# Performance work log

Hardware: AMD Instinct MI355X
Metric: run time of the kernel (lower is better)

Reference implementation:

```python
import jax, jax.numpy as jnp
import numpy as np

NEG_CAUSAL = -1e10  # matches torch buffer triu(ones*-1e10, diag=1)
NEG_PAD = -10000.0
NUM_HEADS = 16


def setup_inputs() -> dict:
    key = jax.random.key(0)
    ks = jax.random.split(key, 6)
    B, S, D = 2, 2048, 1024
    scale = 0.02
    return {
        "hidden_states": jax.random.normal(ks[0], (B, S, D), jnp.float32),
        "attention_mask": jnp.ones((B, S), jnp.float32),
        "Wq": jax.random.normal(ks[1], (D, D), jnp.float32) * scale,
        "bq": jnp.zeros((D,), jnp.float32),
        "Wk": jax.random.normal(ks[2], (D, D), jnp.float32) * scale,
        "bk": jnp.zeros((D,), jnp.float32),
        "Wv": jax.random.normal(ks[3], (D, D), jnp.float32) * scale,
        "bv": jnp.zeros((D,), jnp.float32),
        "Wo": jax.random.normal(ks[4], (D, D), jnp.float32) * scale,
        "bo": jnp.zeros((D,), jnp.float32),
    }


def reference(hidden_states, attention_mask, Wq, bq, Wk, bk, Wv, bv, Wo, bo):
    B, S, D = hidden_states.shape
    H = NUM_HEADS
    hd = D // H

    def heads(x):  # [B,S,D] -> [B,H,S,hd]
        return x.reshape(B, S, H, hd).transpose(0, 2, 1, 3)

    q = heads(hidden_states @ Wq + bq)
    k = heads(hidden_states @ Wk + bk)
    v = heads(hidden_states @ Wv + bv)

    scores = jnp.einsum("bhqd,bhkd->bhqk", q, k) / jnp.sqrt(jnp.float32(hd))
    causal = jnp.triu(jnp.full((S, S), NEG_CAUSAL, jnp.float32), k=1)
    scores = scores + causal
    # additive padding mask: (1 - m) * -10000, broadcast over heads and query pos
    scores = scores + (1.0 - attention_mask)[:, None, None, :] * NEG_PAD

    probs = jax.nn.softmax(scores, axis=-1)
    # dropout p=0.1 is inactive in eval mode (training=False)
    ctx = jnp.einsum("bhqk,bhkd->bhqd", probs, v)
    ctx = ctx.transpose(0, 2, 1, 3).reshape(B, S, D)
    return ctx @ Wo + bo
```

## Files before the change

kernel.cpp:

```cpp
#include <hip/hip_runtime.h>

typedef __attribute__((ext_vector_type(8))) short short8_t;
typedef __attribute__((ext_vector_type(4))) float float4_t;
typedef unsigned short u16;
typedef unsigned int u32;
typedef unsigned long long u64;

__device__ inline u16 f2bf(float x) {
  union { float f; u32 u; } v; v.f = x;
  u32 r = v.u + 0x7FFFu + ((v.u >> 16) & 1u);
  return (u16)(r >> 16);
}
#if __has_builtin(__builtin_amdgcn_cvt_pk_bf16_f32)
typedef __attribute__((ext_vector_type(2))) __bf16 bf162_t;
__device__ inline u32 pk2(float a, float b) {
  union { bf162_t v; u32 u; } cv;
  cv.v = __builtin_amdgcn_cvt_pk_bf16_f32(a, b);
  return cv.u;
}
#else
__device__ inline u32 pk2(float a, float b) {
  return (u32)f2bf(a) | ((u32)f2bf(b) << 16);
}
#endif

__global__ __launch_bounds__(256) void prologue(const float* __restrict__ X,
                                                const float* __restrict__ Wq, const float* __restrict__ Wk,
                                                const float* __restrict__ Wv, const float* __restrict__ Wo,
                                                u16* __restrict__ Xb, u16* __restrict__ WqkvT,
                                                u16* __restrict__ WoT) {
  __shared__ float tls[32][33];
  int bid = blockIdx.x;
  if (bid < 4096) {
    int i = bid * 256 + threadIdx.x;
    float4_t x = ((const float4_t*)X)[i];
    union { u32 u[2]; u64 ll; } o;
    o.u[0] = pk2(x[0], x[1]);
    o.u[1] = pk2(x[2], x[3]);
    ((u64*)Xb)[i] = o.ll;
  } else {
    int t = bid - 4096;
    int mat = t >> 10, tile = t & 1023;
    const float* W = (mat == 0) ? Wq : (mat == 1) ? Wk : (mat == 2) ? Wv : Wo;
    u16* WT = (mat < 3) ? WqkvT + ((size_t)mat << 20) : WoT;
    int tx = threadIdx.x & 31, ty = threadIdx.x >> 5;
    int c0 = (tile & 31) * 32, r0 = (tile >> 5) * 32;
    #pragma unroll
    for (int i = 0; i < 4; ++i)
      tls[ty + i * 8][tx] = W[(r0 + ty + i * 8) * 1024 + c0 + tx];
    __syncthreads();
    #pragma unroll
    for (int i = 0; i < 4; ++i)
      WT[(size_t)(c0 + ty + i * 8) * 1024 + r0 + tx] = f2bf(tls[tx][ty + i * 8]);
  }
}

__global__ __launch_bounds__(256) void gemm128(const u16* __restrict__ A, const u16* __restrict__ BT,
                                               const float* __restrict__ bias0, const float* __restrict__ bias1,
                                               const float* __restrict__ bias2,
                                               void* __restrict__ o0, void* __restrict__ o1, void* __restrict__ o2,
                                               int mode) {
  __shared__ __align__(16) u16 Als[128 * 64];
  __shared__ __align__(16) u16 Bls[128 * 64];
  int g = blockIdx.x, m0t, n0t;
  if (mode == 4) {
    int mh = g / 384, r = g - mh * 384;
    n0t = r >> 4;
    m0t = mh * 16 + (r & 15);
  } else {
    m0t = g & 31;
    n0t = g >> 5;
  }
  const int m0 = m0t * 128, n0 = n0t * 128;
  const int lane = threadIdx.x & 63, wave = threadIdx.x >> 6;
  const int quad = lane >> 4, c = lane & 15;
  const int wm = wave >> 1, wn = wave & 1;

  const int srow = lane >> 3, schunk = lane & 7;
  int soff[4], dst[4];
  #pragma unroll
  for (int q = 0; q < 4; ++q) {
    int r = wave * 32 + q * 8 + srow;
    soff[q] = r * 1024 + (schunk << 3);
    dst[q]  = r * 64 + ((schunk ^ (r & 7)) << 3);
  }
  const u16* gA = A + (size_t)m0 * 1024;
  const u16* gB = BT + (size_t)n0 * 1024;

  int ar[2][4], br[2][4];
  #pragma unroll
  for (int ko = 0; ko < 2; ++ko) {
    #pragma unroll
    for (int i = 0; i < 4; ++i) {
      int rowa = wm * 64 + i * 16 + c;
      ar[ko][i] = rowa * 64 + (((ko * 4 + quad) ^ (rowa & 7)) << 3);
      int rowb = wn * 64 + i * 16 + c;
      br[ko][i] = rowb * 64 + (((ko * 4 + quad) ^ (rowb & 7)) << 3);
    }
  }

  short8_t ra[4], rb[4];
  #pragma unroll
  for (int q = 0; q < 4; ++q) ra[q] = *(const short8_t*)(gA + soff[q]);
  #pragma unroll
  for (int q = 0; q < 4; ++q) rb[q] = *(const short8_t*)(gB + soff[q]);

  float4_t acc[4][4] = {};
  for (int k0 = 0; k0 < 1024; k0 += 64) {
    #pragma unroll
    for (int q = 0; q < 4; ++q) *(short8_t*)&Als[dst[q]] = ra[q];
    #pragma unroll
    for (int q = 0; q < 4; ++q) *(short8_t*)&Bls[dst[q]] = rb[q];
    __syncthreads();
    if (k0 < 960) {
      #pragma unroll
      for (int q = 0; q < 4; ++q) ra[q] = *(const short8_t*)(gA + soff[q] + k0 + 64);
      #pragma unroll
      for (int q = 0; q < 4; ++q) rb[q] = *(const short8_t*)(gB + soff[q] + k0 + 64);
    }
    #pragma unroll
    for (int ko = 0; ko < 2; ++ko) {
      short8_t af[4], bfr[4];
      #pragma unroll
      for (int i = 0; i < 4; ++i) af[i] = *(const short8_t*)&Als[ar[ko][i]];
      #pragma unroll
      for (int j = 0; j < 4; ++j) bfr[j] = *(const short8_t*)&Bls[br[ko][j]];
      #pragma unroll
      for (int i = 0; i < 4; ++i)
        #pragma unroll
        for (int j = 0; j < 4; ++j)
          acc[i][j] = __builtin_amdgcn_mfma_f32_16x16x32_bf16(af[i], bfr[j], acc[i][j], 0, 0, 0);
    }
    __syncthreads();
  }

  const int mrow = m0 + wm * 64, ncol = n0 + wn * 64;
  if (mode == 3) {
    float* o = (float*)o0;
    #pragma unroll
    for (int i = 0; i < 4; ++i) {
      #pragma unroll
      for (int j = 0; j < 4; ++j) {
        int colb = ncol + j * 16 + c;
        float bv = bias0[colb];
        int rowb = mrow + i * 16 + quad * 4;
        #pragma unroll
        for (int r = 0; r < 4; ++r)
          o[(size_t)(rowb + r) * 1024 + colb] = acc[i][j][r] + bv;
      }
    }
  } else {
    #pragma unroll
    for (int j = 0; j < 4; ++j) {
      int colb = ncol + j * 16 + c;
      int which = colb >> 10;
      int n1 = colb & 1023, h = n1 >> 6, d = n1 & 63;
      const float* bp = (which == 0) ? bias0 : (which == 1 ? bias1 : bias2);
      float bv = bp[n1];
      #pragma unroll
      for (int i = 0; i < 4; ++i) {
        int rowb = mrow + i * 16 + quad * 4;
        int b = rowb >> 11, s = rowb & 2047;
        if (which == 2) {
          u16* o = (u16*)o2 + (((size_t)(b * 16 + h) * 64 + d) * 2048 + s);
          union { u32 u[2]; u64 ll; } ov;
          ov.u[0] = pk2(acc[i][j][0] + bv, acc[i][j][1] + bv);
          ov.u[1] = pk2(acc[i][j][2] + bv, acc[i][j][3] + bv);
          *(u64*)o = ov.ll;
        } else {
          float sc = (which == 0) ? 0.125f : 1.0f;
          u16* o = (u16*)((which == 0) ? o0 : o1);
          #pragma unroll
          for (int r = 0; r < 4; ++r)
            o[(((size_t)(b * 16 + h) * 2048 + (s + r)) << 6) + d] = f2bf((acc[i][j][r] + bv) * sc);
        }
      }
    }
  }
}

__device__ inline short8_t p_to_b32(const float* p, int quad, int c) {
  u32 pk0[2] = {pk2(p[0], p[1]), pk2(p[2], p[3])};
  u32 pk1[2] = {pk2(p[4], p[5]), pk2(p[6], p[7])};
  int base = ((quad & 1) * 2) * 16 + c;
  union { u32 u[4]; short8_t v; } pf;
  #pragma unroll
  for (int x = 0; x < 4; ++x) {
    int src = base + ((x >> 1) << 4);
    int v0 = __shfl((int)pk0[x & 1], src);
    int v1 = __shfl((int)pk1[x & 1], src);
    pf.u[x] = (quad < 2) ? (u32)v0 : (u32)v1;
  }
  return pf.v;
}

__global__ __launch_bounds__(256, 4) void attn_kernel(const u16* __restrict__ Q, const u16* __restrict__ K,
                                                      const u16* __restrict__ VT, const float* __restrict__ mask,
                                                      u16* __restrict__ ctx) {
  __shared__ __align__(16) u16 Kls[2 * 64 * 64];
  __shared__ __align__(16) u16 Vls[2 * 64 * 64];
  const float C1 = 10000.0f * 1.4426950408889634f;
  const float LOG2E = 1.4426950408889634f;
  int w = threadIdx.x >> 6, lane = threadIdx.x & 63;
  int quad = lane >> 4, c = lane & 15;
  int g = blockIdx.x;
  int bh = (g & 7) * 4 + ((g >> 3) & 3);
  int u = g >> 5;
  int qt = (u < 16) ? (31 - u) : (u - 16);
  int b = bh >> 4, h = bh & 15;
  const u16* Kp = K + ((size_t)bh << 17);
  const u16* Vp = VT + ((size_t)bh << 17);
  const float* mp = mask + (b << 11);
  int q0 = qt * 64 + w * 16;

  const u16* Qp = Q + (((size_t)bh * 2048 + q0 + c) << 6) + quad * 8;
  short8_t qf0 = *(const short8_t*)(Qp);
  short8_t qf1 = *(const short8_t*)(Qp + 32);

  const int srow = lane >> 3, schunk = lane & 7;
  const u16* gK[2]; const u16* gV[2]; int dK[2], dV[2];
  #pragma unroll
  for (int i = 0; i < 2; ++i) {
    int R = w * 16 + i * 8 + srow;
    gK[i] = Kp + R * 64 + (schunk << 3);
    dK[i] = R * 64 + ((schunk ^ (R & 7)) << 3);
    gV[i] = Vp + (size_t)R * 2048 + (schunk << 3);
    dV[i] = R * 64 + ((schunk ^ (R & 7)) << 3);
  }

  int koff[4][2];
  #pragma unroll
  for (int kg = 0; kg < 4; ++kg) {
    int r = kg * 16 + c;
    #pragma unroll
    for (int ko = 0; ko < 2; ++ko)
      koff[kg][ko] = r * 64 + (((ko * 4 + quad) ^ (r & 7)) << 3);
  }
  int voff[4][2];
  #pragma unroll
  for (int dblk = 0; dblk < 4; ++dblk) {
    int d = dblk * 16 + c;
    #pragma unroll
    for (int kc = 0; kc < 2; ++kc)
      voff[dblk][kc] = d * 64 + (((kc * 4 + quad) ^ (d & 7)) << 3);
  }

  int ke[8];
  #pragma unroll
  for (int e = 0; e < 8; ++e) ke[e] = ((e >> 2) << 4) + quad * 4 + (e & 3);
  int thr = w * 16 + c;

  float4_t O[4] = {};
  float l = 0.0f;

  short8_t kreg[2], vreg[2];
  #pragma unroll
  for (int i = 0; i < 2; ++i) { kreg[i] = *(const short8_t*)(gK[i]); vreg[i] = *(const short8_t*)(gV[i]); }

  for (int t = 0; t <= qt; ++t) {
    int kb = t << 6;
    int bufo = (t & 1) << 12;
    #pragma unroll
    for (int i = 0; i < 2; ++i) *(short8_t*)&Kls[bufo + dK[i]] = kreg[i];
    #pragma unroll
    for (int i = 0; i < 2; ++i) *(short8_t*)&Vls[bufo + dV[i]] = vreg[i];
    __syncthreads();
    if (t < qt) {
      int kb2 = (t + 1) << 6;
      #pragma unroll
      for (int i = 0; i < 2; ++i) {
        kreg[i] = *(const short8_t*)(gK[i] + (size_t)kb2 * 64);
        vreg[i] = *(const short8_t*)(gV[i] + kb2);
      }
    }
    float4_t s[4];
    #pragma unroll
    for (int kg = 0; kg < 4; ++kg) {
      short8_t k0 = *(const short8_t*)&Kls[bufo + koff[kg][0]];
      short8_t k1 = *(const short8_t*)&Kls[bufo + koff[kg][1]];
      float4_t a = {};
      a = __builtin_amdgcn_mfma_f32_16x16x32_bf16(k0, qf0, a, 0, 0, 0);
      a = __builtin_amdgcn_mfma_f32_16x16x32_bf16(k1, qf1, a, 0, 0, 0);
      s[kg] = a;
    }
    float4_t mpl[4];
    #pragma unroll
    for (int kg = 0; kg < 4; ++kg)
      mpl[kg] = (*(const float4_t*)(mp + kb + kg * 16 + quad * 4) - 1.0f) * C1;
    bool diag = (t == qt);
    short8_t pf[2];
    #pragma unroll
    for (int kc = 0; kc < 2; ++kc) {
      float p[8];
      #pragma unroll
      for (int e = 0; e < 8; ++e) {
        int kg = kc * 2 + (e >> 2);
        p[e] = __builtin_fmaf(s[kg][e & 3], LOG2E, mpl[kg][e & 3]);
      }
      if (diag) {
        #pragma unroll
        for (int e = 0; e < 8; ++e) {
          int ko2 = kc * 32 + ke[e];
          p[e] = (ko2 > thr) ? -50.0f : p[e];
        }
      }
      #pragma unroll
      for (int e = 0; e < 8; ++e) {
        float pe = exp2f(p[e]);
        p[e] = pe;
        l += pe;
      }
      pf[kc] = p_to_b32(p, quad, c);
    }
    #pragma unroll
    for (int dblk = 0; dblk < 4; ++dblk) {
      #pragma unroll
      for (int kc = 0; kc < 2; ++kc) {
        short8_t vf = *(const short8_t*)&Vls[bufo + voff[dblk][kc]];
        O[dblk] = __builtin_amdgcn_mfma_f32_16x16x32_bf16(vf, pf[kc], O[dblk], 0, 0, 0);
      }
    }
  }
  l += __shfl_xor(l, 16);
  l += __shfl_xor(l, 32);
  float rl = 1.0f / l;
  u16* op = ctx + ((size_t)(b * 2048 + q0 + c) * 1024 + h * 64 + quad * 4);
  #pragma unroll
  for (int dblk = 0; dblk < 4; ++dblk) {
    union { u32 uu[2]; u64 ll; } ov;
    ov.uu[0] = pk2(O[dblk][0] * rl, O[dblk][1] * rl);
    ov.uu[1] = pk2(O[dblk][2] * rl, O[dblk][3] * rl);
    *(u64*)(op + dblk * 16) = ov.ll;
  }
}

extern "C" void kernel_launch(void* const* d_in, const int* in_sizes, int n_in,
                              void* d_out, int out_size, void* d_ws, size_t ws_size,
                              hipStream_t stream) {
  const float* X    = (const float*)d_in[0];
  const float* mask = (const float*)d_in[1];
  const float* Wq   = (const float*)d_in[2];
  const float* bq   = (const float*)d_in[3];
  const float* Wk   = (const float*)d_in[4];
  const float* bk   = (const float*)d_in[5];
  const float* Wv   = (const float*)d_in[6];
  const float* bv   = (const float*)d_in[7];
  const float* Wo   = (const float*)d_in[8];
  const float* bo   = (const float*)d_in[9];

  char* w = (char*)d_ws;
  u16* Xb     = (u16*)(w);
  u16* WqkvT  = (u16*)(w + (8ull  << 20));
  u16* WoT    = (u16*)(w + (14ull << 20));
  u16* Qb     = (u16*)(w + (16ull << 20));
  u16* Kb     = (u16*)(w + (24ull << 20));
  u16* VTb    = (u16*)(w + (32ull << 20));
  u16* Ctx    = (u16*)(w + (40ull << 20));

  prologue<<<8192, 256, 0, stream>>>(X, Wq, Wk, Wv, Wo, Xb, WqkvT, WoT);
  gemm128<<<768, 256, 0, stream>>>(Xb, WqkvT, bq, bk, bv, Qb, Kb, VTb, 4);
  attn_kernel<<<1024, 256, 0, stream>>>(Qb, Kb, VTb, mask, Ctx);
  gemm128<<<256, 256, 0, stream>>>(Ctx, WoT, bo, bo, bo, d_out, d_out, d_out, 3);
}
```

Baseline: 201.6 us.

## Split attention KV range across wave pairs, load K/V directly, skip all-ones mask

The attention kernel now runs each 16-query group on two waves that each take half of the causal KV range. Their partial outputs and row sums are merged through shared memory. K and V fragments are read straight from global memory, which removes the shared-memory staging and the per-tile barrier. The prologue adds a per-batch flag that marks an all-ones mask so the mask add can be skipped, and log2(e) is folded into the Q scale in the QKV GEMM epilogue. In exchange the grid is twice as large, global reads are uncoalesced and repeated across waves, and the kernel depends on the workspace being large enough to hold the flags.

```diff
diff --git a/kernel.cpp b/kernel.cpp
--- a/kernel.cpp
+++ b/kernel.cpp
@@ -28,7 +28,8 @@
                                                 const float* __restrict__ Wq, const float* __restrict__ Wk,
                                                 const float* __restrict__ Wv, const float* __restrict__ Wo,
                                                 u16* __restrict__ Xb, u16* __restrict__ WqkvT,
-                                                u16* __restrict__ WoT) {
+                                                u16* __restrict__ WoT, const float* __restrict__ maskp,
+                                                u32* __restrict__ flags) {
   __shared__ float tls[32][33];
   int bid = blockIdx.x;
   if (bid < 4096) {
@@ -38,7 +39,7 @@
     o.u[0] = pk2(x[0], x[1]);
     o.u[1] = pk2(x[2], x[3]);
     ((u64*)Xb)[i] = o.ll;
-  } else {
+  } else if (bid < 8192) {
     int t = bid - 4096;
     int mat = t >> 10, tile = t & 1023;
     const float* W = (mat == 0) ? Wq : (mat == 1) ? Wk : (mat == 2) ? Wv : Wo;
@@ -52,6 +53,19 @@
     #pragma unroll
     for (int i = 0; i < 4; ++i)
       WT[(size_t)(c0 + ty + i * 8) * 1024 + r0 + tx] = f2bf(tls[tx][ty + i * 8]);
+  } else {
+    int b = bid - 8192;
+    const float* mb = maskp + (b << 11) + threadIdx.x * 8;
+    bool ok = true;
+    #pragma unroll
+    for (int i = 0; i < 8; ++i) ok &= (mb[i] == 1.0f);
+    u64 bal = __ballot(ok);
+    int w = threadIdx.x >> 6;
+    if ((threadIdx.x & 63) == 0) tls[0][w] = (bal == ~0ull) ? 1.0f : 0.0f;
+    __syncthreads();
+    if (threadIdx.x == 0)
+      flags[b] = (tls[0][0] != 0.0f && tls[0][1] != 0.0f &&
+                  tls[0][2] != 0.0f && tls[0][3] != 0.0f) ? 1u : 0u;
   }
 }
 
@@ -168,7 +182,7 @@
           ov.u[1] = pk2(acc[i][j][2] + bv, acc[i][j][3] + bv);
           *(u64*)o = ov.ll;
         } else {
-          float sc = (which == 0) ? 0.125f : 1.0f;
+          float sc = (which == 0) ? 0.18033688011112042f : 1.0f;
           u16* o = (u16*)((which == 0) ? o0 : o1);
           #pragma unroll
           for (int r = 0; r < 4; ++r)
@@ -194,100 +208,66 @@
   return pf.v;
 }
 
-__global__ __launch_bounds__(256, 4) void attn_kernel(const u16* __restrict__ Q, const u16* __restrict__ K,
+__global__ __launch_bounds__(256, 6) void attn_kernel(const u16* __restrict__ Q, const u16* __restrict__ K,
                                                       const u16* __restrict__ VT, const float* __restrict__ mask,
-                                                      u16* __restrict__ ctx) {
-  __shared__ __align__(16) u16 Kls[2 * 64 * 64];
-  __shared__ __align__(16) u16 Vls[2 * 64 * 64];
+                                                      const u32* __restrict__ flags, u16* __restrict__ ctx) {
+  __shared__ float Ols[2][64][17];
+  __shared__ float Lls[2][16];
   const float C1 = 10000.0f * 1.4426950408889634f;
-  const float LOG2E = 1.4426950408889634f;
   int w = threadIdx.x >> 6, lane = threadIdx.x & 63;
   int quad = lane >> 4, c = lane & 15;
   int g = blockIdx.x;
   int bh = (g & 7) * 4 + ((g >> 3) & 3);
   int u = g >> 5;
-  int qt = (u < 16) ? (31 - u) : (u - 16);
+  int m = 31 - (u >> 1);
+  int p2 = u & 1;
+  int pr = w >> 1, half = w & 1;
+  int jj = p2 * 2 + pr;
+  int j = (m << 2) + jj;
   int b = bh >> 4, h = bh & 15;
+  bool ones = flags && (flags[b] != 0);
+
   const u16* Kp = K + ((size_t)bh << 17);
   const u16* Vp = VT + ((size_t)bh << 17);
   const float* mp = mask + (b << 11);
-  int q0 = qt * 64 + w * 16;
-
-  const u16* Qp = Q + (((size_t)bh * 2048 + q0 + c) << 6) + quad * 8;
+
+  const u16* Qp = Q + (((size_t)bh * 2048 + j * 16 + c) << 6) + quad * 8;
   short8_t qf0 = *(const short8_t*)(Qp);
   short8_t qf1 = *(const short8_t*)(Qp + 32);
 
-  const int srow = lane >> 3, schunk = lane & 7;
-  const u16* gK[2]; const u16* gV[2]; int dK[2], dV[2];
-  #pragma unroll
-  for (int i = 0; i < 2; ++i) {
-    int R = w * 16 + i * 8 + srow;
-    gK[i] = Kp + R * 64 + (schunk << 3);
-    dK[i] = R * 64 + ((schunk ^ (R & 7)) << 3);
-    gV[i] = Vp + (size_t)R * 2048 + (schunk << 3);
-    dV[i] = R * 64 + ((schunk ^ (R & 7)) << 3);
-  }
-
-  int koff[4][2];
-  #pragma unroll
-  for (int kg = 0; kg < 4; ++kg) {
-    int r = kg * 16 + c;
-    #pragma unroll
-    for (int ko = 0; ko < 2; ++ko)
-      koff[kg][ko] = r * 64 + (((ko * 4 + quad) ^ (r & 7)) << 3);
-  }
-  int voff[4][2];
-  #pragma unroll
-  for (int dblk = 0; dblk < 4; ++dblk) {
-    int d = dblk * 16 + c;
-    #pragma unroll
-    for (int kc = 0; kc < 2; ++kc)
-      voff[dblk][kc] = d * 64 + (((kc * 4 + quad) ^ (d & 7)) << 3);
-  }
-
-  int ke[8];
-  #pragma unroll
-  for (int e = 0; e < 8; ++e) ke[e] = ((e >> 2) << 4) + quad * 4 + (e & 3);
-  int thr = w * 16 + c;
+  const u16* kb0 = Kp + c * 64 + quad * 8;
+  const u16* vb0 = Vp + c * 2048 + quad * 8;
+
+  int n = m + 1, h0 = n >> 1;
+  int lo = half ? h0 : 0, hi = half ? n : h0;
+  int tq = jj * 16 + c - quad * 4;
 
   float4_t O[4] = {};
   float l = 0.0f;
 
-  short8_t kreg[2], vreg[2];
-  #pragma unroll
-  for (int i = 0; i < 2; ++i) { kreg[i] = *(const short8_t*)(gK[i]); vreg[i] = *(const short8_t*)(gV[i]); }
-
-  for (int t = 0; t <= qt; ++t) {
+  for (int t = lo; t < hi; ++t) {
     int kb = t << 6;
-    int bufo = (t & 1) << 12;
-    #pragma unroll
-    for (int i = 0; i < 2; ++i) *(short8_t*)&Kls[bufo + dK[i]] = kreg[i];
-    #pragma unroll
-    for (int i = 0; i < 2; ++i) *(short8_t*)&Vls[bufo + dV[i]] = vreg[i];
-    __syncthreads();
-    if (t < qt) {
-      int kb2 = (t + 1) << 6;
-      #pragma unroll
-      for (int i = 0; i < 2; ++i) {
-        kreg[i] = *(const short8_t*)(gK[i] + (size_t)kb2 * 64);
-        vreg[i] = *(const short8_t*)(gV[i] + kb2);
-      }
-    }
+    short8_t kf[4][2];
+    #pragma unroll
+    for (int kg = 0; kg < 4; ++kg)
+      #pragma unroll
+      for (int ko = 0; ko < 2; ++ko)
+        kf[kg][ko] = *(const short8_t*)(kb0 + (kb + kg * 16) * 64 + ko * 32);
     float4_t s[4];
     #pragma unroll
     for (int kg = 0; kg < 4; ++kg) {
-      short8_t k0 = *(const short8_t*)&Kls[bufo + koff[kg][0]];
-      short8_t k1 = *(const short8_t*)&Kls[bufo + koff[kg][1]];
       float4_t a = {};
-      a = __builtin_amdgcn_mfma_f32_16x16x32_bf16(k0, qf0, a, 0, 0, 0);
-      a = __builtin_amdgcn_mfma_f32_16x16x32_bf16(k1, qf1, a, 0, 0, 0);
+      a = __builtin_amdgcn_mfma_f32_16x16x32_bf16(kf[kg][0], qf0, a, 0, 0, 0);
+      a = __builtin_amdgcn_mfma_f32_16x16x32_bf16(kf[kg][1], qf1, a, 0, 0, 0);
       s[kg] = a;
     }
     float4_t mpl[4];
-    #pragma unroll
-    for (int kg = 0; kg < 4; ++kg)
-      mpl[kg] = (*(const float4_t*)(mp + kb + kg * 16 + quad * 4) - 1.0f) * C1;
-    bool diag = (t == qt);
+    if (!ones) {
+      #pragma unroll
+      for (int kg = 0; kg < 4; ++kg)
+        mpl[kg] = (*(const float4_t*)(mp + kb + kg * 16 + quad * 4) - 1.0f) * C1;
+    }
+    bool diag = (t == m);
     short8_t pf[2];
     #pragma unroll
     for (int kc = 0; kc < 2; ++kc) {
@@ -295,13 +275,14 @@
       #pragma unroll
       for (int e = 0; e < 8; ++e) {
         int kg = kc * 2 + (e >> 2);
-        p[e] = __builtin_fmaf(s[kg][e & 3], LOG2E, mpl[kg][e & 3]);
+        p[e] = s[kg][e & 3];
+        if (!ones) p[e] += mpl[kg][e & 3];
       }
       if (diag) {
         #pragma unroll
         for (int e = 0; e < 8; ++e) {
-          int ko2 = kc * 32 + ke[e];
-          p[e] = (ko2 > thr) ? -50.0f : p[e];
+          int Ce = kc * 32 + ((e >> 2) << 4) + (e & 3);
+          p[e] = (Ce > tq) ? -50.0f : p[e];
         }
       }
       #pragma unroll
@@ -314,22 +295,36 @@
     }
     #pragma unroll
     for (int dblk = 0; dblk < 4; ++dblk) {
-      #pragma unroll
-      for (int kc = 0; kc < 2; ++kc) {
-        short8_t vf = *(const short8_t*)&Vls[bufo + voff[dblk][kc]];
-        O[dblk] = __builtin_amdgcn_mfma_f32_16x16x32_bf16(vf, pf[kc], O[dblk], 0, 0, 0);
-      }
-    }
-  }
+      short8_t v0 = *(const short8_t*)(vb0 + dblk * 16 * 2048 + kb);
+      short8_t v1 = *(const short8_t*)(vb0 + dblk * 16 * 2048 + kb + 32);
+      O[dblk] = __builtin_amdgcn_mfma_f32_16x16x32_bf16(v0, pf[0], O[dblk], 0, 0, 0);
+      O[dblk] = __builtin_amdgcn_mfma_f32_16x16x32_bf16(v1, pf[1], O[dblk], 0, 0, 0);
+    }
+  }
+
   l += __shfl_xor(l, 16);
   l += __shfl_xor(l, 32);
-  float rl = 1.0f / l;
-  u16* op = ctx + ((size_t)(b * 2048 + q0 + c) * 1024 + h * 64 + quad * 4);
+  if (half) {
+    #pragma unroll
+    for (int dblk = 0; dblk < 4; ++dblk)
+      #pragma unroll
+      for (int r = 0; r < 4; ++r)
+        Ols[pr][dblk * 16 + quad * 4 + r][c] = O[dblk][r];
+    if (quad == 0) Lls[pr][c] = l;
+  }
+  __syncthreads();
+  if (half) return;
+  float rl = 1.0f / (l + Lls[pr][c]);
+  u16* op = ctx + ((size_t)(b * 2048 + j * 16 + c) * 1024 + h * 64 + quad * 4);
   #pragma unroll
   for (int dblk = 0; dblk < 4; ++dblk) {
+    float o0v = (O[dblk][0] + Ols[pr][dblk * 16 + quad * 4 + 0][c]) * rl;
+    float o1v = (O[dblk][1] + Ols[pr][dblk * 16 + quad * 4 + 1][c]) * rl;
+    float o2v = (O[dblk][2] + Ols[pr][dblk * 16 + quad * 4 + 2][c]) * rl;
+    float o3v = (O[dblk][3] + Ols[pr][dblk * 16 + quad * 4 + 3][c]) * rl;
     union { u32 uu[2]; u64 ll; } ov;
-    ov.uu[0] = pk2(O[dblk][0] * rl, O[dblk][1] * rl);
-    ov.uu[1] = pk2(O[dblk][2] * rl, O[dblk][3] * rl);
+    ov.uu[0] = pk2(o0v, o1v);
+    ov.uu[1] = pk2(o2v, o3v);
     *(u64*)(op + dblk * 16) = ov.ll;
   }
 }
@@ -356,9 +351,10 @@
   u16* Kb     = (u16*)(w + (24ull << 20));
   u16* VTb    = (u16*)(w + (32ull << 20));
   u16* Ctx    = (u16*)(w + (40ull << 20));
-
-  prologue<<<8192, 256, 0, stream>>>(X, Wq, Wk, Wv, Wo, Xb, WqkvT, WoT);
+  u32* flags  = (ws_size >= (48ull << 20) + 8) ? (u32*)(w + (48ull << 20)) : nullptr;
+
+  prologue<<<flags ? 8194 : 8192, 256, 0, stream>>>(X, Wq, Wk, Wv, Wo, Xb, WqkvT, WoT, mask, flags);
   gemm128<<<768, 256, 0, stream>>>(Xb, WqkvT, bq, bk, bv, Qb, Kb, VTb, 4);
-  attn_kernel<<<1024, 256, 0, stream>>>(Qb, Kb, VTb, mask, Ctx);
+  attn_kernel<<<2048, 256, 0, stream>>>(Qb, Kb, VTb, mask, flags, Ctx);
   gemm128<<<256, 256, 0, stream>>>(Ctx, WoT, bo, bo, bo, d_out, d_out, d_out, 3);
 }
```

Result: slower. 294.6 us (+46.1%).

## Skip padding-mask loads when all ones, fold log2e into Q, use permlane swaps

Applied to the files above, without the earlier changes.

The prologue gains two blocks that check whether each batch's attention mask is all ones and write a per-batch flag. The attention kernel reads the flag and skips the per-tile mask loads and adds when it is set. The log2e factor is folded into the Q scale in the QKV GEMM epilogue, which removes a multiply per score. The shuffle-based P-to-B-fragment repack is replaced with v_permlane32/16_swap instructions. The mask check is a real runtime test, so the general path is kept, but the flag depends on the workspace being large enough.

```diff
diff --git a/kernel.cpp b/kernel.cpp
--- a/kernel.cpp
+++ b/kernel.cpp
@@ -28,7 +28,8 @@
                                                 const float* __restrict__ Wq, const float* __restrict__ Wk,
                                                 const float* __restrict__ Wv, const float* __restrict__ Wo,
                                                 u16* __restrict__ Xb, u16* __restrict__ WqkvT,
-                                                u16* __restrict__ WoT) {
+                                                u16* __restrict__ WoT, const float* __restrict__ maskp,
+                                                u32* __restrict__ flags) {
   __shared__ float tls[32][33];
   int bid = blockIdx.x;
   if (bid < 4096) {
@@ -38,7 +39,7 @@
     o.u[0] = pk2(x[0], x[1]);
     o.u[1] = pk2(x[2], x[3]);
     ((u64*)Xb)[i] = o.ll;
-  } else {
+  } else if (bid < 8192) {
     int t = bid - 4096;
     int mat = t >> 10, tile = t & 1023;
     const float* W = (mat == 0) ? Wq : (mat == 1) ? Wk : (mat == 2) ? Wv : Wo;
@@ -52,6 +53,19 @@
     #pragma unroll
     for (int i = 0; i < 4; ++i)
       WT[(size_t)(c0 + ty + i * 8) * 1024 + r0 + tx] = f2bf(tls[tx][ty + i * 8]);
+  } else {
+    int b = bid - 8192;
+    const float* mb = maskp + (b << 11) + threadIdx.x * 8;
+    bool ok = true;
+    #pragma unroll
+    for (int i = 0; i < 8; ++i) ok &= (mb[i] == 1.0f);
+    u64 bal = __ballot(ok);
+    int w = threadIdx.x >> 6;
+    if ((threadIdx.x & 63) == 0) tls[0][w] = (bal == ~0ull) ? 1.0f : 0.0f;
+    __syncthreads();
+    if (threadIdx.x == 0)
+      flags[b] = (tls[0][0] != 0.0f && tls[0][1] != 0.0f &&
+                  tls[0][2] != 0.0f && tls[0][3] != 0.0f) ? 1u : 0u;
   }
 }
 
@@ -168,7 +182,7 @@
           ov.u[1] = pk2(acc[i][j][2] + bv, acc[i][j][3] + bv);
           *(u64*)o = ov.ll;
         } else {
-          float sc = (which == 0) ? 0.125f : 1.0f;
+          float sc = (which == 0) ? 0.18033688011112042f : 1.0f;
           u16* o = (u16*)((which == 0) ? o0 : o1);
           #pragma unroll
           for (int r = 0; r < 4; ++r)
@@ -179,28 +193,24 @@
   }
 }
 
-__device__ inline short8_t p_to_b32(const float* p, int quad, int c) {
-  u32 pk0[2] = {pk2(p[0], p[1]), pk2(p[2], p[3])};
-  u32 pk1[2] = {pk2(p[4], p[5]), pk2(p[6], p[7])};
-  int base = ((quad & 1) * 2) * 16 + c;
+__device__ inline short8_t p_to_b_swap(const float* p) {
+  u32 a0 = pk2(p[0], p[1]), a1 = pk2(p[2], p[3]);
+  u32 b0 = pk2(p[4], p[5]), b1 = pk2(p[6], p[7]);
+  asm("v_permlane32_swap_b32 %0, %1" : "+v"(a0), "+v"(b0));
+  asm("v_permlane32_swap_b32 %0, %1" : "+v"(a1), "+v"(b1));
+  asm("v_permlane16_swap_b32 %0, %1" : "+v"(a0), "+v"(b0));
+  asm("v_permlane16_swap_b32 %0, %1" : "+v"(a1), "+v"(b1));
   union { u32 u[4]; short8_t v; } pf;
-  #pragma unroll
-  for (int x = 0; x < 4; ++x) {
-    int src = base + ((x >> 1) << 4);
-    int v0 = __shfl((int)pk0[x & 1], src);
-    int v1 = __shfl((int)pk1[x & 1], src);
-    pf.u[x] = (quad < 2) ? (u32)v0 : (u32)v1;
-  }
+  pf.u[0] = a0; pf.u[1] = a1; pf.u[2] = b0; pf.u[3] = b1;
   return pf.v;
 }
 
 __global__ __launch_bounds__(256, 4) void attn_kernel(const u16* __restrict__ Q, const u16* __restrict__ K,
                                                       const u16* __restrict__ VT, const float* __restrict__ mask,
-                                                      u16* __restrict__ ctx) {
+                                                      const u32* __restrict__ flags, u16* __restrict__ ctx) {
   __shared__ __align__(16) u16 Kls[2 * 64 * 64];
   __shared__ __align__(16) u16 Vls[2 * 64 * 64];
   const float C1 = 10000.0f * 1.4426950408889634f;
-  const float LOG2E = 1.4426950408889634f;
   int w = threadIdx.x >> 6, lane = threadIdx.x & 63;
   int quad = lane >> 4, c = lane & 15;
   int g = blockIdx.x;
@@ -208,6 +218,7 @@
   int u = g >> 5;
   int qt = (u < 16) ? (31 - u) : (u - 16);
   int b = bh >> 4, h = bh & 15;
+  bool ones = flags && (flags[b] != 0);
   const u16* Kp = K + ((size_t)bh << 17);
   const u16* Vp = VT + ((size_t)bh << 17);
   const float* mp = mask + (b << 11);
@@ -284,9 +295,11 @@
       s[kg] = a;
     }
     float4_t mpl[4];
-    #pragma unroll
-    for (int kg = 0; kg < 4; ++kg)
-      mpl[kg] = (*(const float4_t*)(mp + kb + kg * 16 + quad * 4) - 1.0f) * C1;
+    if (!ones) {
+      #pragma unroll
+      for (int kg = 0; kg < 4; ++kg)
+        mpl[kg] = (*(const float4_t*)(mp + kb + kg * 16 + quad * 4) - 1.0f) * C1;
+    }
     bool diag = (t == qt);
     short8_t pf[2];
     #pragma unroll
@@ -295,7 +308,8 @@
       #pragma unroll
       for (int e = 0; e < 8; ++e) {
         int kg = kc * 2 + (e >> 2);
-        p[e] = __builtin_fmaf(s[kg][e & 3], LOG2E, mpl[kg][e & 3]);
+        p[e] = s[kg][e & 3];
+        if (!ones) p[e] += mpl[kg][e & 3];
       }
       if (diag) {
         #pragma unroll
@@ -310,7 +324,7 @@
         p[e] = pe;
         l += pe;
       }
-      pf[kc] = p_to_b32(p, quad, c);
+      pf[kc] = p_to_b_swap(p);
     }
     #pragma unroll
     for (int dblk = 0; dblk < 4; ++dblk) {
@@ -356,9 +370,10 @@
   u16* Kb     = (u16*)(w + (24ull << 20));
   u16* VTb    = (u16*)(w + (32ull << 20));
   u16* Ctx    = (u16*)(w + (40ull << 20));
-
-  prologue<<<8192, 256, 0, stream>>>(X, Wq, Wk, Wv, Wo, Xb, WqkvT, WoT);
+  u32* flags  = (ws_size >= (48ull << 20) + 8) ? (u32*)(w + (48ull << 20)) : nullptr;
+
+  prologue<<<flags ? 8194 : 8192, 256, 0, stream>>>(X, Wq, Wk, Wv, Wo, Xb, WqkvT, WoT, mask, flags);
   gemm128<<<768, 256, 0, stream>>>(Xb, WqkvT, bq, bk, bv, Qb, Kb, VTb, 4);
-  attn_kernel<<<1024, 256, 0, stream>>>(Qb, Kb, VTb, mask, Ctx);
+  attn_kernel<<<1024, 256, 0, stream>>>(Qb, Kb, VTb, mask, flags, Ctx);
   gemm128<<<256, 256, 0, stream>>>(Ctx, WoT, bo, bo, bo, d_out, d_out, d_out, 3);
 }
```

New measurement: 185.7 us. 1.09x faster.
